# Kernel tuning notes

Measured on AMD Instinct MI355X. Metric: run time of the kernel, lower is better.

Reference implementation:

```python
import math
import jax, jax.numpy as jnp
import numpy as np

D_MODEL = 1024
D_CTX = 1024
NUM_HEADS = 16
ATTN_DIM = 1024
HEAD_DIM = ATTN_DIM // NUM_HEADS  # 64
ROPE_GAMMA = 10.0
ROTARY_BASE = 10000.0
ATTN_SCALE = math.sqrt(ATTN_DIM)  # note: module scales by sqrt(attn_dim), not sqrt(head_dim)


def _apply_rope(x, cos, sin):
    # x: [H,B,T,D]; cos/sin: [1,B,T,D//2]
    half = x.shape[-1] // 2
    x1, x2 = x[..., :half], x[..., half:]
    return jnp.concatenate([x1 * cos - x2 * sin, x1 * sin + x2 * cos], axis=-1)


def setup_inputs() -> dict:
    key = jax.random.key(0)
    ks = jax.random.split(key, 12)
    B, T, L = 4, 1024, 1024
    x = jax.random.normal(ks[0], (B, D_MODEL, T), jnp.float32)
    context = jax.random.normal(ks[1], (B, L, D_CTX), jnp.float32)
    # prefix (padding) masks with per-example valid lengths, as in real padded batches
    lens_q = jnp.array([1024, 896, 768, 640])
    lens_k = jnp.array([1024, 960, 832, 704])
    x_mask = (jnp.arange(T)[None, :] < lens_q[:, None]).astype(jnp.int32)[:, None, :]  # [B,1,T]
    context_mask = (jnp.arange(L)[None, :] < lens_k[:, None]).astype(jnp.int32)[:, None, :]  # [B,1,L]
    s = 0.02
    Wq = jax.random.normal(ks[2], (D_MODEL, ATTN_DIM), jnp.float32) * s
    bq = jax.random.normal(ks[3], (ATTN_DIM,), jnp.float32) * s
    Wk = jax.random.normal(ks[4], (D_CTX, ATTN_DIM), jnp.float32) * s
    bk = jax.random.normal(ks[5], (ATTN_DIM,), jnp.float32) * s
    Wv = jax.random.normal(ks[6], (D_CTX, ATTN_DIM), jnp.float32) * s
    bv = jax.random.normal(ks[7], (ATTN_DIM,), jnp.float32) * s
    Wo = jax.random.normal(ks[8], (ATTN_DIM, D_MODEL), jnp.float32) * s
    bo = jax.random.normal(ks[9], (D_MODEL,), jnp.float32) * s
    return {"x": x, "context": context, "x_mask": x_mask, "context_mask": context_mask,
            "Wq": Wq, "bq": bq, "Wk": Wk, "bk": bk, "Wv": Wv, "bv": bv, "Wo": Wo, "bo": bo}


def reference(x, context, x_mask, context_mask, Wq, bq, Wk, bk, Wv, bv, Wo, bo):
    B, _, T = x.shape
    L = context.shape[1]
    H, D = NUM_HEADS, HEAD_DIM
    xm = x_mask.astype(jnp.float32)          # [B,1,T]
    cmf = context_mask.astype(jnp.float32)   # [B,1,L]

    q = jnp.swapaxes(x, 1, 2) @ Wq + bq      # [B,T,attn_dim]
    k = context @ Wk + bk                    # [B,L,attn_dim]
    v = context @ Wv + bv                    # [B,L,attn_dim]

    q = q.reshape(B, T, H, D).transpose(2, 0, 1, 3)  # [H,B,T,D]
    k = k.reshape(B, L, H, D).transpose(2, 0, 1, 3)  # [H,B,L,D]
    v = v.reshape(B, L, H, D).transpose(2, 0, 1, 3)  # [H,B,L,D]

    # length-normalized RoPE (LARoPE)
    len_q = xm.sum(axis=(-2, -1)).reshape(-1, 1, 1)   # [B,1,1]
    len_k = cmf.sum(axis=(-2, -1)).reshape(-1, 1, 1)  # [B,1,1]
    pos_q = jnp.arange(T, dtype=jnp.float32).reshape(1, -1, 1)
    pos_k = jnp.arange(L, dtype=jnp.float32).reshape(1, -1, 1)
    inv_freq = 1.0 / (ROTARY_BASE ** (jnp.arange(0, D, 2, dtype=jnp.float32) / D))
    theta = (inv_freq * ROPE_GAMMA).reshape(1, 1, -1)  # [1,1,D//2]
    freqs_q = (pos_q / len_q) * theta  # [B,T,D//2]
    freqs_k = (pos_k / len_k) * theta  # [B,L,D//2]
    q = _apply_rope(q, jnp.cos(freqs_q)[None], jnp.sin(freqs_q)[None])
    k = _apply_rope(k, jnp.cos(freqs_k)[None], jnp.sin(freqs_k)[None])

    logits = jnp.einsum('hbtd,hbld->hbtl', q, k) / ATTN_SCALE  # [H,B,T,L]
    key_pad = (context_mask == 0)[None]  # [1,B,1,L]
    logits = jnp.where(key_pad, -jnp.inf, logits)
    attn = jax.nn.softmax(logits, axis=-1)
    query_pad = (x_mask == 0).transpose(1, 0, 2)[..., None]  # [1,B,T,1]
    attn = jnp.where(query_pad, 0.0, attn)

    out = jnp.einsum('hbtl,hbld->hbtd', attn, v)          # [H,B,T,D]
    out = out.transpose(1, 2, 0, 3).reshape(B, T, ATTN_DIM)
    out = out @ Wo + bo                                   # [B,T,d_model]
    out = out * jnp.swapaxes(xm, 1, 2)                    # [B,T,1] broadcast
    return jnp.swapaxes(out, 1, 2)                        # [B,d_model,T]
```

## Files before the change

kernel.cpp:

```cpp
#include <hip/hip_runtime.h>
#include <hip/hip_bf16.h>

typedef __attribute__((ext_vector_type(8))) short s8v;
typedef __attribute__((ext_vector_type(4))) float f4v;
typedef __attribute__((ext_vector_type(4))) unsigned short u4v;
typedef __attribute__((ext_vector_type(2))) unsigned int u2v;

#define NH 16

__device__ __forceinline__ unsigned short f2bf(float f) {
  union { float f; unsigned int u; } v; v.f = f;
  unsigned int r = (v.u + 0x7fffu + ((v.u >> 16) & 1u)) >> 16;
  return (unsigned short)r;
}
__device__ __forceinline__ void gll16(const void* g, void* l) {
  __builtin_amdgcn_global_load_lds((const __attribute__((address_space(1))) void*)g,
                                   (__attribute__((address_space(3))) void*)l, 16, 0, 0);
}
__device__ __forceinline__ unsigned int cvtpk(float lo, float hi) {
  unsigned int r;
  asm volatile("v_cvt_pk_bf16_f32 %0, %1, %2" : "=v"(r) : "v"(lo), "v"(hi));
  return r;
}

__global__ __launch_bounds__(256) void prep_kernel(
    const float* __restrict__ x, const float* __restrict__ ctx,
    const float* __restrict__ Wq, const float* __restrict__ Wk,
    const float* __restrict__ Wv, const float* __restrict__ Wo,
    const int* __restrict__ xm, const int* __restrict__ cm,
    unsigned short* __restrict__ xT, unsigned short* __restrict__ ctxb,
    unsigned short* __restrict__ WqT, unsigned short* __restrict__ WkT,
    unsigned short* __restrict__ WvT, unsigned short* __restrict__ WoT,
    float* __restrict__ lens, float2* __restrict__ rope) {
  const int z = blockIdx.z;
  const int tid = threadIdx.x;
  if (z == 12) {
    if (blockIdx.x | blockIdx.y) return;
    const int w = tid >> 6, lane = tid & 63;
    const int g = w * 2 + (lane >> 5);
    const int l32 = lane & 31;
    const int* m = (g < 4) ? (xm + g * 1024) : (cm + (g - 4) * 1024);
    int s = 0;
    for (int i = l32; i < 1024; i += 32) s += m[i];
    for (int o = 16; o; o >>= 1) s += __shfl_xor(s, o);
    if (l32 == 0) lens[g] = (float)s;
    return;
  }
  if (z == 13) {
    const int idx = blockIdx.y * 32 + blockIdx.x;
    if (idx >= 256) return;
    const int which = idx >> 7;
    const int b = (idx >> 5) & 3;
    const int t0 = (idx & 31) * 32;
    const int* m = (which ? cm : xm) + b * 1024;
    const int lane = tid & 63;
    int s = 0;
    for (int i = lane; i < 1024; i += 64) s += m[i];
    for (int o = 32; o; o >>= 1) s += __shfl_xor(s, o);
    const float len = (float)s;
    const int j = tid & 31;
    const float theta = 10.0f * __expf((float)j * -0.28782313662425572f);
    float2* rt = rope + ((size_t)(which * 4 + b) << 15);
    for (int it = 0; it < 4; ++it) {
      const int t = t0 + (tid >> 5) + it * 8;
      const float fr = (float)t / len * theta;
      float sn, cs;
      __sincosf(fr, &sn, &cs);
      rt[t * 32 + j] = make_float2(cs, sn);
    }
    return;
  }
  if (z >= 8) {
    const float* in = ctx + ((size_t)(z - 8) << 20);
    unsigned short* out = ctxb + ((size_t)(z - 8) << 20);
    const int i = (blockIdx.y * 32 + blockIdx.x) * 1024 + tid * 4;
    const f4v v = *(const f4v*)&in[i];
    u4v o;
#pragma unroll
    for (int j = 0; j < 4; ++j) o[j] = f2bf(v[j]);
    *(u4v*)&out[i] = o;
    return;
  }
  __shared__ unsigned short tile[32][33];
  const float* in;
  unsigned short* out;
  if (z < 4)      { in = x + ((size_t)z << 20); out = xT + ((size_t)z << 20); }
  else if (z == 4){ in = Wq; out = WqT; }
  else if (z == 5){ in = Wk; out = WkT; }
  else if (z == 6){ in = Wv; out = WvT; }
  else            { in = Wo; out = WoT; }
  const int r0 = blockIdx.y * 32, c0 = blockIdx.x * 32;
  const int tx = tid & 31, ty = tid >> 5;
  for (int i = ty; i < 32; i += 8) tile[i][tx] = f2bf(in[(size_t)(r0 + i) * 1024 + c0 + tx]);
  __syncthreads();
  for (int i = ty; i < 32; i += 8) out[(size_t)(c0 + i) * 1024 + r0 + tx] = tile[tx][i];
}

#define STAGE_QKV(buf, kt_) do {                                         \
    const int kn_ = (kt_) * 64;                                          \
    _Pragma("unroll")                                                    \
    for (int i_ = 0; i_ < 4; ++i_) {                                     \
      gll16(Ap + i_ * 32 * 1024 + kn_, &As[buf][(i_ * 256 + tid) * 8]);  \
      gll16(Bp + i_ * 32 * 1024 + kn_, &Bs[buf][(i_ * 256 + tid) * 8]);  \
    }                                                                    \
  } while (0)

__global__ __launch_bounds__(256) void gemm_qkv_kernel(
    const unsigned short* __restrict__ xT, const unsigned short* __restrict__ ctxb,
    const unsigned short* __restrict__ WqT, const unsigned short* __restrict__ WkT,
    const unsigned short* __restrict__ WvT,
    const float* __restrict__ bq, const float* __restrict__ bk, const float* __restrict__ bv,
    unsigned short* __restrict__ Qb, unsigned short* __restrict__ Kb,
    unsigned short* __restrict__ Vtb, const float2* __restrict__ rope,
    const float* __restrict__ lens) {
  __shared__ __attribute__((aligned(16))) unsigned short As[2][8192];
  __shared__ __attribute__((aligned(16))) unsigned short Bs[2][8192];
  const int id = blockIdx.x + (blockIdx.y << 3) + (blockIdx.z << 8);
  const int rest = id >> 3;
  const int my = (id & 7) + ((rest & 3) << 3);
  const int nx = (rest >> 2) & 7;
  const int mode = rest >> 5;
  const int b = my >> 3;
  const int lim = (int)lens[(mode == 0 ? 0 : 4) + b];
  if (((my & 7) << 7) >= lim) return;
  const unsigned short* A  = (mode == 0) ? xT : ctxb;
  const unsigned short* Bt = (mode == 0) ? WqT : (mode == 1) ? WkT : WvT;
  const float* bias        = (mode == 0) ? bq : (mode == 1) ? bk : bv;
  const int tid = threadIdx.x;
  const int lane = tid & 63, w = tid >> 6;
  const int lq = lane & 15, lg = lane >> 4;
  const int m0 = my * 128, n0 = nx * 128;
  const int wm = (w & 1) * 64, wn = (w >> 1) * 64;
  const int cswz = (lq & 7) << 3;
  const int srow = tid >> 3;
  const int scol = ((tid & 7) * 8) ^ ((srow & 7) << 3);
  const unsigned short* Ap = A + (size_t)(m0 + srow) * 1024 + scol;
  const unsigned short* Bp = Bt + (size_t)(n0 + srow) * 1024 + scol;
  f4v acc[4][4] = {};

  STAGE_QKV(0, 0);
  STAGE_QKV(1, 1);

  for (int kt = 0; kt < 16; ++kt) {
    const int cur = kt & 1;
    if (kt < 15) {
      asm volatile("s_waitcnt vmcnt(8)" ::: "memory");
    } else {
      asm volatile("s_waitcnt vmcnt(0)" ::: "memory");
    }
    __builtin_amdgcn_s_barrier();
#pragma unroll
    for (int kc = 0; kc < 2; ++kc) {
      s8v af[4], bfr[4];
#pragma unroll
      for (int i = 0; i < 4; ++i)
        af[i] = *(const s8v*)&As[cur][(wm + i * 16 + lq) * 64 + ((kc * 32 + lg * 8) ^ cswz)];
#pragma unroll
      for (int i = 0; i < 4; ++i)
        bfr[i] = *(const s8v*)&Bs[cur][(wn + i * 16 + lq) * 64 + ((kc * 32 + lg * 8) ^ cswz)];
#pragma unroll
      for (int mi = 0; mi < 4; ++mi)
#pragma unroll
        for (int ni = 0; ni < 4; ++ni)
          acc[mi][ni] = __builtin_amdgcn_mfma_f32_16x16x32_bf16(af[mi], bfr[ni], acc[mi][ni], 0, 0, 0);
    }
    __builtin_amdgcn_s_barrier();
    if (kt + 2 < 16) STAGE_QKV(cur, kt + 2);
  }

  float bv4[4];
#pragma unroll
  for (int ni = 0; ni < 4; ++ni) bv4[ni] = bias[n0 + wn + ni * 16 + lq];

  if (mode <= 1) {
    unsigned short* O = mode ? Kb : Qb;
    const float osc = mode ? 1.0f : 0.0450842200277f;
    const float2* rt = rope + ((size_t)(mode * 4 + b) << 15);
    const int h = (n0 + wn) >> 6;
#pragma unroll
    for (int mi = 0; mi < 4; ++mi) {
#pragma unroll
      for (int rr = 0; rr < 4; ++rr) {
        const int m = m0 + wm + mi * 16 + lg * 4 + rr;
        const int t = m & 1023;
#pragma unroll
        for (int ni = 0; ni < 2; ++ni) {
          const int jj = ni * 16 + lq;
          const float2 cs2 = rt[t * 32 + jj];
          const float x1 = acc[mi][ni][rr] + bv4[ni];
          const float x2 = acc[mi][ni + 2][rr] + bv4[ni + 2];
          unsigned short* bp = &O[((size_t)((b * NH + h) * 1024 + t)) * 64 + jj];
          bp[0] = f2bf((x1 * cs2.x - x2 * cs2.y) * osc);
          bp[32] = f2bf((x1 * cs2.y + x2 * cs2.x) * osc);
        }
      }
    }
  } else {
#pragma unroll
    for (int mi = 0; mi < 4; ++mi) {
      const int mbase = m0 + wm + mi * 16 + lg * 4;
      const int l0 = mbase & 1023;
#pragma unroll
      for (int ni = 0; ni < 4; ++ni) {
        const int n = n0 + wn + ni * 16 + lq;
        const int hh = n >> 6, d = n & 63;
        u4v pk;
#pragma unroll
        for (int rr = 0; rr < 4; ++rr) pk[rr] = f2bf(acc[mi][ni][rr] + bv4[ni]);
        *(u4v*)&Vtb[((size_t)((b * NH + hh) * 64 + d)) * 1024 + l0] = pk;
      }
    }
  }
}

__global__ __launch_bounds__(256) void gemm_o_kernel(
    const unsigned short* __restrict__ A, const unsigned short* __restrict__ Bt,
    const float* __restrict__ bias, float* __restrict__ Cout,
    const int* __restrict__ xmask, const float* __restrict__ lens) {
  __shared__ __attribute__((aligned(16))) unsigned short As[2][8192];
  __shared__ __attribute__((aligned(16))) unsigned short Bs[2][8192];
  const int id = blockIdx.x + (blockIdx.y << 3);
  const int rest = id >> 3;
  const int my = (id & 7) + ((rest & 3) << 3);
  const int nx = rest >> 2;
  const int tid = threadIdx.x;
  const int lane = tid & 63, w = tid >> 6;
  const int lq = lane & 15, lg = lane >> 4;
  const int m0 = my * 128, n0 = nx * 128;
  const int wm = (w & 1) * 64, wn = (w >> 1) * 64;
  const int b = my >> 3;

  if (((my & 7) << 7) >= (int)lens[b]) {
#pragma unroll
    for (int mi = 0; mi < 4; ++mi) {
      const int t0 = (m0 + wm + mi * 16 + lg * 4) & 1023;
      const f4v z = {};
#pragma unroll
      for (int ni = 0; ni < 4; ++ni) {
        const int n = n0 + wn + ni * 16 + lq;
        *(f4v*)&Cout[(size_t)b * 1024 * 1024 + (size_t)n * 1024 + t0] = z;
      }
    }
    return;
  }

  const int cswz = (lq & 7) << 3;
  const int srow = tid >> 3;
  const int scol = ((tid & 7) * 8) ^ ((srow & 7) << 3);
  const unsigned short* Ap = A + (size_t)(m0 + srow) * 1024 + scol;
  const unsigned short* Bp = Bt + (size_t)(n0 + srow) * 1024 + scol;
  f4v acc[4][4] = {};

  STAGE_QKV(0, 0);
  STAGE_QKV(1, 1);

  for (int kt = 0; kt < 16; ++kt) {
    const int cur = kt & 1;
    if (kt < 15) {
      asm volatile("s_waitcnt vmcnt(8)" ::: "memory");
    } else {
      asm volatile("s_waitcnt vmcnt(0)" ::: "memory");
    }
    __builtin_amdgcn_s_barrier();
#pragma unroll
    for (int kc = 0; kc < 2; ++kc) {
      s8v af[4], bfr[4];
#pragma unroll
      for (int i = 0; i < 4; ++i)
        af[i] = *(const s8v*)&As[cur][(wm + i * 16 + lq) * 64 + ((kc * 32 + lg * 8) ^ cswz)];
#pragma unroll
      for (int i = 0; i < 4; ++i)
        bfr[i] = *(const s8v*)&Bs[cur][(wn + i * 16 + lq) * 64 + ((kc * 32 + lg * 8) ^ cswz)];
#pragma unroll
      for (int mi = 0; mi < 4; ++mi)
#pragma unroll
        for (int ni = 0; ni < 4; ++ni)
          acc[mi][ni] = __builtin_amdgcn_mfma_f32_16x16x32_bf16(af[mi], bfr[ni], acc[mi][ni], 0, 0, 0);
    }
    __builtin_amdgcn_s_barrier();
    if (kt + 2 < 16) STAGE_QKV(cur, kt + 2);
  }

  float bv4[4];
#pragma unroll
  for (int ni = 0; ni < 4; ++ni) bv4[ni] = bias[n0 + wn + ni * 16 + lq];
#pragma unroll
  for (int mi = 0; mi < 4; ++mi) {
    const int mbase = m0 + wm + mi * 16 + lg * 4;
    const int t0 = mbase & 1023;
#pragma unroll
    for (int ni = 0; ni < 4; ++ni) {
      const int n = n0 + wn + ni * 16 + lq;
      f4v pk;
#pragma unroll
      for (int rr = 0; rr < 4; ++rr) {
        float v = acc[mi][ni][rr] + bv4[ni];
        v *= (float)xmask[b * 1024 + t0 + rr];
        pk[rr] = v;
      }
      *(f4v*)&Cout[(size_t)b * 1024 * 1024 + (size_t)n * 1024 + t0] = pk;
    }
  }
}

__global__ __launch_bounds__(512) void attn_kernel(
    const unsigned short* __restrict__ Q, const unsigned short* __restrict__ K,
    const unsigned short* __restrict__ Vt, const float* __restrict__ lens,
    unsigned short* __restrict__ Aout) {
  __shared__ __attribute__((aligned(16))) unsigned short Ks[2][4096];
  __shared__ __attribute__((aligned(16))) unsigned short Vs[2][4096];
  __shared__ __attribute__((aligned(16))) unsigned short Plds[8][16][72];
  const int tid = threadIdx.x;
  const int lane = tid & 63, w = tid >> 6;
  const int lq = lane & 15, lg = lane >> 4;
  const int id = blockIdx.x + (blockIdx.y << 3);
  const int bh = (id & 7) + (((id >> 3) & 7) << 3);
  const int qblk = id >> 6;
  const int b = bh >> 4, h = bh & 15;
  const int lenq = (int)lens[b];
  if (qblk * 128 >= lenq) return;
  const int lenk = (int)lens[4 + b];
  const int nkt = (lenk + 63) >> 6;
  const int qrow = qblk * 128 + w * 16;
  const unsigned short* Qp = Q + ((size_t)bh * 1024 + qrow) * 64;
  const unsigned short* Kp = K + (size_t)bh * 65536;
  const unsigned short* Vp = Vt + (size_t)bh * 65536;
  const s8v qf0 = *(const s8v*)&Qp[lq * 64 + lg * 8];
  const s8v qf1 = *(const s8v*)&Qp[lq * 64 + 32 + lg * 8];
  const int r0 = tid >> 3;
  const int c0x = ((tid & 7) * 8) ^ ((r0 & 7) << 3);
  const int cswz = (lq & 7) << 3;

  gll16(&Kp[(size_t)r0 * 64 + c0x], &Ks[0][tid * 8]);
  gll16(&Vp[(size_t)r0 * 1024 + c0x], &Vs[0][tid * 8]);
  __syncthreads();

  float s_run = 0.0f;
  f4v ot[4] = {};
  for (int kt = 0; kt < nkt; ++kt) {
    const int p = kt & 1;
    if (kt + 1 < nkt) {
      const int kn = (kt + 1) * 64;
      gll16(&Kp[(size_t)(kn + r0) * 64 + c0x], &Ks[p ^ 1][tid * 8]);
      gll16(&Vp[(size_t)r0 * 1024 + kn + c0x], &Vs[p ^ 1][tid * 8]);
    }
    const int k0 = kt * 64;
    const bool full = (k0 + 64 <= lenk);
    float pvv[16];
    __builtin_amdgcn_s_setprio(1);
#pragma unroll
    for (int kk = 0; kk < 4; ++kk) {
      const int krow = kk * 16 + lq;
      const s8v a0 = *(const s8v*)&Ks[p][krow * 64 + ((lg * 8) ^ cswz)];
      const s8v a1 = *(const s8v*)&Ks[p][krow * 64 + ((32 + lg * 8) ^ cswz)];
      f4v s = {};
      s = __builtin_amdgcn_mfma_f32_16x16x32_bf16(a0, qf0, s, 0, 0, 0);
      s = __builtin_amdgcn_mfma_f32_16x16x32_bf16(a1, qf1, s, 0, 0, 0);
#pragma unroll
      for (int rr = 0; rr < 4; ++rr) {
        float v = s[rr];
        if (!full) {
          const int key = k0 + kk * 16 + lg * 4 + rr;
          if (key >= lenk) v = -1e30f;
        }
        pvv[kk * 4 + rr] = v;
      }
    }
    __builtin_amdgcn_s_setprio(0);
#pragma unroll
    for (int kk = 0; kk < 4; ++kk) {
      const float e0 = exp2f(pvv[kk * 4 + 0]);
      const float e1 = exp2f(pvv[kk * 4 + 1]);
      const float e2 = exp2f(pvv[kk * 4 + 2]);
      const float e3 = exp2f(pvv[kk * 4 + 3]);
      s_run += (e0 + e1) + (e2 + e3);
      u2v pw;
      pw[0] = cvtpk(e0, e1);
      pw[1] = cvtpk(e2, e3);
      *(u2v*)&Plds[w][lq][kk * 16 + lg * 4] = pw;
    }
    const s8v pb0 = *(const s8v*)&Plds[w][lq][lg * 8];
    const s8v pb1 = *(const s8v*)&Plds[w][lq][32 + lg * 8];
    __builtin_amdgcn_s_setprio(1);
#pragma unroll
    for (int d = 0; d < 4; ++d) {
      const int vrow = d * 16 + lq;
      const s8v av0 = *(const s8v*)&Vs[p][vrow * 64 + ((lg * 8) ^ cswz)];
      const s8v av1 = *(const s8v*)&Vs[p][vrow * 64 + ((32 + lg * 8) ^ cswz)];
      ot[d] = __builtin_amdgcn_mfma_f32_16x16x32_bf16(av0, pb0, ot[d], 0, 0, 0);
      ot[d] = __builtin_amdgcn_mfma_f32_16x16x32_bf16(av1, pb1, ot[d], 0, 0, 0);
    }
    __builtin_amdgcn_s_setprio(0);
    if (kt + 1 < nkt) __syncthreads();
  }
  s_run += __shfl_xor(s_run, 16);
  s_run += __shfl_xor(s_run, 32);
  const float inv = 1.0f / s_run;
  const int t = qrow + lq;
  unsigned short* op = Aout + ((size_t)(b * 1024 + t)) * 1024 + h * 64;
#pragma unroll
  for (int d = 0; d < 4; ++d) {
    u4v oo;
#pragma unroll
    for (int rr = 0; rr < 4; ++rr) oo[rr] = f2bf(ot[d][rr] * inv);
    *(u4v*)&op[d * 16 + lg * 4] = oo;
  }
}

extern "C" void kernel_launch(void* const* d_in, const int* in_sizes, int n_in,
                              void* d_out, int out_size, void* d_ws, size_t ws_size,
                              hipStream_t stream) {
  const float* x   = (const float*)d_in[0];
  const float* ctx = (const float*)d_in[1];
  const int* xm = (const int*)d_in[2];
  const int* cm = (const int*)d_in[3];
  const float* Wq = (const float*)d_in[4];
  const float* bq = (const float*)d_in[5];
  const float* Wk = (const float*)d_in[6];
  const float* bk = (const float*)d_in[7];
  const float* Wv = (const float*)d_in[8];
  const float* bv = (const float*)d_in[9];
  const float* Wo = (const float*)d_in[10];
  const float* bo = (const float*)d_in[11];

  char* ws = (char*)d_ws;
  const size_t MB = 1024 * 1024;
  unsigned short* xT   = (unsigned short*)(ws);
  unsigned short* AOb  = (unsigned short*)(ws);
  unsigned short* ctxb = (unsigned short*)(ws + 8 * MB);
  unsigned short* WqT  = (unsigned short*)(ws + 16 * MB);
  unsigned short* WkT  = (unsigned short*)(ws + 18 * MB);
  unsigned short* WvT  = (unsigned short*)(ws + 20 * MB);
  unsigned short* WoT  = (unsigned short*)(ws + 22 * MB);
  unsigned short* Qb   = (unsigned short*)(ws + 24 * MB);
  unsigned short* Kb   = (unsigned short*)(ws + 32 * MB);
  unsigned short* Vtb  = (unsigned short*)(ws + 40 * MB);
  float* lens          = (float*)(ws + 48 * MB);
  float2* rope         = (float2*)(ws + 49 * MB);

  prep_kernel<<<dim3(32, 32, 14), 256, 0, stream>>>(x, ctx, Wq, Wk, Wv, Wo, xm, cm,
                                                    xT, ctxb, WqT, WkT, WvT, WoT, lens, rope);
  gemm_qkv_kernel<<<dim3(8, 32, 3), 256, 0, stream>>>(xT, ctxb, WqT, WkT, WvT,
                                                      bq, bk, bv, Qb, Kb, Vtb, rope, lens);
  attn_kernel<<<dim3(8, 64), 512, 0, stream>>>(Qb, Kb, Vtb, lens, AOb);
  gemm_o_kernel<<<dim3(8, 32), 256, 0, stream>>>(AOb, WoT, bo, (float*)d_out, xm, lens);
}
```

Baseline: 113.4 us.

## Retile QKV GEMM to 256x256 blocks with 512 threads and 4-stage pipeline

The QKV projection GEMM moves from 128x128 tiles with 256 threads and a double-buffered K=64 loop to 256x256 tiles with 512 threads, K=32 subtiles and a 4-slot LDS ring. A and B loads are interleaved between MFMA halves, and s_setprio raises priority around the MFMA bursts. The goal is more data reuse per block and better overlap of loads with compute. In exchange the grid shrinks to 192 blocks on a large-CU GPU, registers per thread roughly double, and the coarser padding-skip granularity may waste work and lower occupancy.

Measured after the change: 110.6 us. 1.03x faster.

```diff
diff --git a/kernel.cpp b/kernel.cpp
--- a/kernel.cpp
+++ b/kernel.cpp
@@ -96,16 +96,7 @@
   for (int i = ty; i < 32; i += 8) out[(size_t)(c0 + i) * 1024 + r0 + tx] = tile[tx][i];
 }
 
-#define STAGE_QKV(buf, kt_) do {                                         \
-    const int kn_ = (kt_) * 64;                                          \
-    _Pragma("unroll")                                                    \
-    for (int i_ = 0; i_ < 4; ++i_) {                                     \
-      gll16(Ap + i_ * 32 * 1024 + kn_, &As[buf][(i_ * 256 + tid) * 8]);  \
-      gll16(Bp + i_ * 32 * 1024 + kn_, &Bs[buf][(i_ * 256 + tid) * 8]);  \
-    }                                                                    \
-  } while (0)
-
-__global__ __launch_bounds__(256) void gemm_qkv_kernel(
+__global__ __launch_bounds__(512) void gemm_qkv_kernel(
     const unsigned short* __restrict__ xT, const unsigned short* __restrict__ ctxb,
     const unsigned short* __restrict__ WqT, const unsigned short* __restrict__ WkT,
     const unsigned short* __restrict__ WvT,
@@ -113,75 +104,87 @@
     unsigned short* __restrict__ Qb, unsigned short* __restrict__ Kb,
     unsigned short* __restrict__ Vtb, const float2* __restrict__ rope,
     const float* __restrict__ lens) {
-  __shared__ __attribute__((aligned(16))) unsigned short As[2][8192];
-  __shared__ __attribute__((aligned(16))) unsigned short Bs[2][8192];
-  const int id = blockIdx.x + (blockIdx.y << 3) + (blockIdx.z << 8);
-  const int rest = id >> 3;
-  const int my = (id & 7) + ((rest & 3) << 3);
-  const int nx = (rest >> 2) & 7;
-  const int mode = rest >> 5;
-  const int b = my >> 3;
+  __shared__ __attribute__((aligned(16))) unsigned short As[4][8192];
+  __shared__ __attribute__((aligned(16))) unsigned short Bs[4][8192];
+  const int id = blockIdx.x + (blockIdx.y << 3);
+  const int mode = id >> 6;
+  const int r = id & 63;
+  const int my = r & 15;
+  const int nx = r >> 4;
+  const int b = my >> 2;
   const int lim = (int)lens[(mode == 0 ? 0 : 4) + b];
-  if (((my & 7) << 7) >= lim) return;
+  if (((my & 3) << 8) >= lim) return;
   const unsigned short* A  = (mode == 0) ? xT : ctxb;
   const unsigned short* Bt = (mode == 0) ? WqT : (mode == 1) ? WkT : WvT;
   const float* bias        = (mode == 0) ? bq : (mode == 1) ? bk : bv;
   const int tid = threadIdx.x;
   const int lane = tid & 63, w = tid >> 6;
   const int lq = lane & 15, lg = lane >> 4;
-  const int m0 = my * 128, n0 = nx * 128;
-  const int wm = (w & 1) * 64, wn = (w >> 1) * 64;
-  const int cswz = (lq & 7) << 3;
-  const int srow = tid >> 3;
-  const int scol = ((tid & 7) * 8) ^ ((srow & 7) << 3);
-  const unsigned short* Ap = A + (size_t)(m0 + srow) * 1024 + scol;
-  const unsigned short* Bp = Bt + (size_t)(n0 + srow) * 1024 + scol;
-  f4v acc[4][4] = {};
-
-  STAGE_QKV(0, 0);
-  STAGE_QKV(1, 1);
-
-  for (int kt = 0; kt < 16; ++kt) {
-    const int cur = kt & 1;
-    if (kt < 15) {
-      asm volatile("s_waitcnt vmcnt(8)" ::: "memory");
-    } else {
-      asm volatile("s_waitcnt vmcnt(0)" ::: "memory");
-    }
-    __builtin_amdgcn_s_barrier();
-#pragma unroll
-    for (int kc = 0; kc < 2; ++kc) {
-      s8v af[4], bfr[4];
-#pragma unroll
-      for (int i = 0; i < 4; ++i)
-        af[i] = *(const s8v*)&As[cur][(wm + i * 16 + lq) * 64 + ((kc * 32 + lg * 8) ^ cswz)];
-#pragma unroll
-      for (int i = 0; i < 4; ++i)
-        bfr[i] = *(const s8v*)&Bs[cur][(wn + i * 16 + lq) * 64 + ((kc * 32 + lg * 8) ^ cswz)];
-#pragma unroll
-      for (int mi = 0; mi < 4; ++mi)
-#pragma unroll
-        for (int ni = 0; ni < 4; ++ni)
-          acc[mi][ni] = __builtin_amdgcn_mfma_f32_16x16x32_bf16(af[mi], bfr[ni], acc[mi][ni], 0, 0, 0);
-    }
-    __builtin_amdgcn_s_barrier();
-    if (kt + 2 < 16) STAGE_QKV(cur, kt + 2);
-  }
+  const int wm = w & 1, wnq = w >> 1;
+  const int m0 = my * 256, n0 = nx * 256;
+  const int srow = tid >> 2;
+  const int scolx = (((tid & 3) ^ ((tid >> 3) & 3)) << 3);
+  const unsigned short* Ap = A + (size_t)(m0 + srow) * 1024 + scolx;
+  const unsigned short* Bp = Bt + (size_t)(n0 + srow) * 1024 + scolx;
+  const int axor = ((lg ^ ((lq >> 1) & 3)) << 3);
+  const int abase = (wm * 128 + lq) * 32 + axor;
+  const int bbase = (wnq * 64 + lq) * 32 + axor;
+  f4v acc[8][4] = {};
+
+#define STG_A(s_) { gll16(Ap + (s_) * 32, &As[(s_) & 3][tid * 8]);                    \
+                    gll16(Ap + 128 * 1024 + (s_) * 32, &As[(s_) & 3][4096 + tid * 8]); }
+#define STG_B(s_) { gll16(Bp + (s_) * 32, &Bs[(s_) & 3][tid * 8]);                    \
+                    gll16(Bp + 128 * 1024 + (s_) * 32, &Bs[(s_) & 3][4096 + tid * 8]); }
+
+#define SUBT(s_, VMASM, DOSTG) do {                                                    \
+    if (DOSTG) STG_A((s_) + 2);                                                        \
+    asm volatile(VMASM ::: "memory");                                                  \
+    __builtin_amdgcn_s_barrier();                                                      \
+    const unsigned short* as_ = As[(s_) & 3];                                          \
+    const unsigned short* bs_ = Bs[(s_) & 3];                                          \
+    s8v af[4], bfr[4];                                                                 \
+    _Pragma("unroll") for (int i = 0; i < 4; ++i)                                      \
+      af[i] = *(const s8v*)&as_[abase + i * 512];                                      \
+    _Pragma("unroll") for (int i = 0; i < 4; ++i)                                      \
+      bfr[i] = *(const s8v*)&bs_[bbase + i * 512];                                     \
+    __builtin_amdgcn_s_setprio(1);                                                     \
+    _Pragma("unroll") for (int mi = 0; mi < 4; ++mi)                                   \
+      _Pragma("unroll") for (int ni = 0; ni < 4; ++ni)                                 \
+        acc[mi][ni] = __builtin_amdgcn_mfma_f32_16x16x32_bf16(af[mi], bfr[ni], acc[mi][ni], 0, 0, 0); \
+    __builtin_amdgcn_s_setprio(0);                                                     \
+    if (DOSTG) STG_B((s_) + 2);                                                        \
+    _Pragma("unroll") for (int i = 0; i < 4; ++i)                                      \
+      af[i] = *(const s8v*)&as_[abase + 2048 + i * 512];                               \
+    __builtin_amdgcn_s_setprio(1);                                                     \
+    _Pragma("unroll") for (int mi = 0; mi < 4; ++mi)                                   \
+      _Pragma("unroll") for (int ni = 0; ni < 4; ++ni)                                 \
+        acc[4 + mi][ni] = __builtin_amdgcn_mfma_f32_16x16x32_bf16(af[mi], bfr[ni], acc[4 + mi][ni], 0, 0, 0); \
+    __builtin_amdgcn_s_setprio(0);                                                     \
+  } while (0)
+
+  STG_A(0); STG_B(0); STG_A(1); STG_B(1);
+
+  for (int s = 0; s < 30; ++s) SUBT(s, "s_waitcnt vmcnt(6)", 1);
+  SUBT(30, "s_waitcnt vmcnt(4)", 0);
+  SUBT(31, "s_waitcnt vmcnt(0)", 0);
+#undef SUBT
+#undef STG_A
+#undef STG_B
 
   float bv4[4];
 #pragma unroll
-  for (int ni = 0; ni < 4; ++ni) bv4[ni] = bias[n0 + wn + ni * 16 + lq];
+  for (int ni = 0; ni < 4; ++ni) bv4[ni] = bias[n0 + wnq * 64 + ni * 16 + lq];
 
   if (mode <= 1) {
     unsigned short* O = mode ? Kb : Qb;
     const float osc = mode ? 1.0f : 0.0450842200277f;
     const float2* rt = rope + ((size_t)(mode * 4 + b) << 15);
-    const int h = (n0 + wn) >> 6;
-#pragma unroll
-    for (int mi = 0; mi < 4; ++mi) {
+    const int h = (n0 >> 6) + wnq;
+#pragma unroll
+    for (int mi = 0; mi < 8; ++mi) {
 #pragma unroll
       for (int rr = 0; rr < 4; ++rr) {
-        const int m = m0 + wm + mi * 16 + lg * 4 + rr;
+        const int m = m0 + wm * 128 + mi * 16 + lg * 4 + rr;
         const int t = m & 1023;
 #pragma unroll
         for (int ni = 0; ni < 2; ++ni) {
@@ -197,12 +200,12 @@
     }
   } else {
 #pragma unroll
-    for (int mi = 0; mi < 4; ++mi) {
-      const int mbase = m0 + wm + mi * 16 + lg * 4;
+    for (int mi = 0; mi < 8; ++mi) {
+      const int mbase = m0 + wm * 128 + mi * 16 + lg * 4;
       const int l0 = mbase & 1023;
 #pragma unroll
       for (int ni = 0; ni < 4; ++ni) {
-        const int n = n0 + wn + ni * 16 + lq;
+        const int n = n0 + wnq * 64 + ni * 16 + lq;
         const int hh = n >> 6, d = n & 63;
         u4v pk;
 #pragma unroll
@@ -212,6 +215,15 @@
     }
   }
 }
+
+#define STAGE_O(buf, kt_) do {                                           \
+    const int kn_ = (kt_) * 64;                                          \
+    _Pragma("unroll")                                                    \
+    for (int i_ = 0; i_ < 4; ++i_) {                                     \
+      gll16(Ap + i_ * 32 * 1024 + kn_, &As[buf][(i_ * 256 + tid) * 8]);  \
+      gll16(Bp + i_ * 32 * 1024 + kn_, &Bs[buf][(i_ * 256 + tid) * 8]);  \
+    }                                                                    \
+  } while (0)
 
 __global__ __launch_bounds__(256) void gemm_o_kernel(
     const unsigned short* __restrict__ A, const unsigned short* __restrict__ Bt,
@@ -251,8 +263,8 @@
   const unsigned short* Bp = Bt + (size_t)(n0 + srow) * 1024 + scol;
   f4v acc[4][4] = {};
 
-  STAGE_QKV(0, 0);
-  STAGE_QKV(1, 1);
+  STAGE_O(0, 0);
+  STAGE_O(1, 1);
 
   for (int kt = 0; kt < 16; ++kt) {
     const int cur = kt & 1;
@@ -278,7 +290,7 @@
           acc[mi][ni] = __builtin_amdgcn_mfma_f32_16x16x32_bf16(af[mi], bfr[ni], acc[mi][ni], 0, 0, 0);
     }
     __builtin_amdgcn_s_barrier();
-    if (kt + 2 < 16) STAGE_QKV(cur, kt + 2);
+    if (kt + 2 < 16) STAGE_O(cur, kt + 2);
   }
 
   float bv4[4];
@@ -440,8 +452,8 @@
 
   prep_kernel<<<dim3(32, 32, 14), 256, 0, stream>>>(x, ctx, Wq, Wk, Wv, Wo, xm, cm,
                                                     xT, ctxb, WqT, WkT, WvT, WoT, lens, rope);
-  gemm_qkv_kernel<<<dim3(8, 32, 3), 256, 0, stream>>>(xT, ctxb, WqT, WkT, WvT,
-                                                      bq, bk, bv, Qb, Kb, Vtb, rope, lens);
+  gemm_qkv_kernel<<<dim3(8, 24), 512, 0, stream>>>(xT, ctxb, WqT, WkT, WvT,
+                                                   bq, bk, bv, Qb, Kb, Vtb, rope, lens);
   attn_kernel<<<dim3(8, 64), 512, 0, stream>>>(Qb, Kb, Vtb, lens, AOb);
   gemm_o_kernel<<<dim3(8, 32), 256, 0, stream>>>(AOb, WoT, bo, (float*)d_out, xm, lens);
 }
```
